# Kernel optimization log

Hardware: AMD Instinct MI355X
Metric: run time of the kernel (lower is better)

The kernel has to match this reference:

```python
import jax, jax.numpy as jnp
import numpy as np

N_NODES = 100000
N_EDGES = 6400000


def setup_inputs() -> dict:
    key = jax.random.key(0)
    k = jax.random.split(key, 5)
    x = jax.random.normal(k[0], (N_NODES, 4), dtype=jnp.float32)
    edge_index = jax.random.randint(k[1], (2, N_EDGES), 0, N_NODES, dtype=jnp.int32)
    # Glorot-style init for GCN linear weights
    W1 = jax.random.normal(k[2], (4, 16), dtype=jnp.float32) * (1.0 / np.sqrt(4.0))
    b1 = jnp.zeros((16,), dtype=jnp.float32)
    W2 = jax.random.normal(k[3], (16, 2), dtype=jnp.float32) * (1.0 / np.sqrt(16.0))
    b2 = jnp.zeros((2,), dtype=jnp.float32)
    return {"x": x, "edge_index": edge_index, "W1": W1, "b1": b1, "W2": W2, "b2": b2}


def _gcn_conv(x, src, dst, deg_inv_sqrt, W, b):
    """One GCNConv layer: linear transform -> symmetric-normalized scatter-add -> bias.

    src, dst already include self-loops; deg_inv_sqrt precomputed on the
    self-loop-augmented graph (matches PyG GCNConv defaults).
    """
    n = x.shape[0]
    h = x @ W                                   # [N, F_out]
    coef = deg_inv_sqrt[src] * deg_inv_sqrt[dst]  # [E+N]
    msg = h[src] * coef[:, None]                # gather + scale, [E+N, F_out]
    out = jax.ops.segment_sum(msg, dst, num_segments=n)  # scatter-add
    return out + b


def reference(x, edge_index, W1, b1, W2, b2):
    n = x.shape[0]
    loop = jnp.arange(n, dtype=edge_index.dtype)
    src = jnp.concatenate([edge_index[0], loop])  # add self-loops
    dst = jnp.concatenate([edge_index[1], loop])
    deg = jax.ops.segment_sum(jnp.ones_like(dst, dtype=x.dtype), dst, num_segments=n)
    deg_inv_sqrt = jnp.where(deg > 0, jax.lax.rsqrt(deg), 0.0)

    h = jax.nn.relu(_gcn_conv(x, src, dst, deg_inv_sqrt, W1, b1))
    return _gcn_conv(h, src, dst, deg_inv_sqrt, W2, b2)
```

## Files before the change

### kernel.cpp

```cpp
#include <hip/hip_runtime.h>

#define TPB 256
#define CSH 10
#define CN 1024
#define NBC_MAX 128
#define STILE 8192
#define EPT (STILE / TPB)

#define B20 1048576
#define S1F 131072.0f
#define S2F 8192.0f

__device__ __forceinline__ unsigned enc_fx(float v, float scale) {
    int xi = __float2int_rn(v * scale);
    xi = max(-(B20 - 1), min(B20 - 1, xi));
    return (unsigned)(xi + B20);
}

__global__ void k_zero(int* __restrict__ p, int n) {
    int i = blockIdx.x * blockDim.x + threadIdx.x;
    if (i < n) p[i] = 0;
}

__global__ void k_histc(const int* __restrict__ dst, int* __restrict__ bcnt, int E, int NBC) {
    __shared__ int cnt[NBC_MAX];
    if (threadIdx.x < NBC_MAX) cnt[threadIdx.x] = 0;
    __syncthreads();
    int per = (E + gridDim.x - 1) / gridDim.x;
    int s = blockIdx.x * per;
    int e = min(E, s + per);
    for (int i = s + threadIdx.x; i < e; i += TPB)
        atomicAdd(&cnt[dst[i] >> CSH], 1);
    __syncthreads();
    if (threadIdx.x < (unsigned)NBC && cnt[threadIdx.x])
        atomicAdd(&bcnt[threadIdx.x], cnt[threadIdx.x]);
}

__global__ void k_scanc(const int* __restrict__ bcnt, int* __restrict__ bbase,
                        int* __restrict__ cursorB, int NBC) {
    __shared__ int sh[NBC_MAX];
    int t = threadIdx.x;
    if (t < NBC) sh[t] = bcnt[t];
    __syncthreads();
    if (t <= NBC) {
        int sum = 0;
        for (int j = 0; j < t && j < NBC; j++) sum += sh[j];
        if (t < NBC) { bbase[t] = sum; cursorB[t] = sum; }
        else if (t == NBC) bbase[NBC] = sum;
    }
}

__global__ void k_passC(const int* __restrict__ src, const int* __restrict__ dst,
                        int* __restrict__ cursorB, unsigned* __restrict__ packed,
                        int E, int NBC, int epb) {
    __shared__ unsigned stage[STILE];
    __shared__ int cnt[NBC_MAX], lb[NBC_MAX], gb[NBC_MAX];
    int bs = blockIdx.x * epb;
    int be = min(E, bs + epb);
    for (int tb = bs; tb < be; tb += STILE) {
        int te = min(be, tb + STILE);
        if (threadIdx.x < NBC_MAX) cnt[threadIdx.x] = 0;
        __syncthreads();
        unsigned pk[EPT];
        int br[EPT];
#pragma unroll
        for (int u = 0; u < EPT; u++) {
            int i = tb + u * TPB + (int)threadIdx.x;
            br[u] = -1;
            if (i < te) {
                int d = dst[i];
                int b = d >> CSH;
                pk[u] = ((unsigned)src[i] << CSH) | (unsigned)(d & (CN - 1));
                int r = atomicAdd(&cnt[b], 1);
                br[u] = b | (r << 7);
            }
        }
        __syncthreads();
        if (threadIdx.x < (unsigned)NBC) {
            int b = threadIdx.x;
            int sum = 0;
            for (int j = 0; j < b; j++) sum += cnt[j];
            lb[b] = sum;
            gb[b] = atomicAdd(&cursorB[b], cnt[b]);
        }
        __syncthreads();
#pragma unroll
        for (int u = 0; u < EPT; u++) {
            if (br[u] >= 0) {
                int b = br[u] & (NBC_MAX - 1);
                int r = br[u] >> 7;
                stage[lb[b] + r] = pk[u];
            }
        }
        __syncthreads();
        int wid = threadIdx.x >> 6, lane = threadIdx.x & 63;
        for (int b = wid; b < NBC; b += 4) {
            int len = cnt[b], l = lb[b], g = gb[b];
            for (int i = lane; i < len; i += 64)
                packed[g + i] = stage[l + i];
        }
        __syncthreads();
    }
}

__global__ void k_degc(const unsigned* __restrict__ packed, const int* __restrict__ bbase,
                       int* __restrict__ deg, int SD, int N) {
    __shared__ int cnt[CN];
    for (int i = threadIdx.x; i < CN; i += TPB) cnt[i] = 0;
    __syncthreads();
    int b = blockIdx.x / SD, s = blockIdx.x - b * SD;
    int e0 = bbase[b], e1 = bbase[b + 1];
    int len = e1 - e0;
    int ce0 = e0 + (int)((long long)len * s / SD);
    int ce1 = e0 + (int)((long long)len * (s + 1) / SD);
    int e = ce0 + threadIdx.x;
    for (; e + 3 * TPB < ce1; e += 4 * TPB) {
        unsigned p0 = packed[e], p1 = packed[e + TPB], p2 = packed[e + 2 * TPB], p3 = packed[e + 3 * TPB];
        atomicAdd(&cnt[p0 & (CN - 1)], 1);
        atomicAdd(&cnt[p1 & (CN - 1)], 1);
        atomicAdd(&cnt[p2 & (CN - 1)], 1);
        atomicAdd(&cnt[p3 & (CN - 1)], 1);
    }
    for (; e < ce1; e += TPB)
        atomicAdd(&cnt[packed[e] & (CN - 1)], 1);
    __syncthreads();
    int node0 = b << CSH;
    for (int i = threadIdx.x; i < CN; i += TPB)
        if (cnt[i] && node0 + i < N) atomicAdd(&deg[node0 + i], cnt[i]);
}

__global__ void k_prepv(const float* __restrict__ x, const int* __restrict__ deg,
                        float* __restrict__ xs, unsigned* __restrict__ xse, int N) {
    int v = blockIdx.x * blockDim.x + threadIdx.x;
    if (v >= N) return;
    float di = rsqrtf((float)(deg[v] + 1));
    float4 xv = ((const float4*)x)[v];
    xv.x *= di; xv.y *= di; xv.z *= di; xv.w *= di;
    ((float4*)xs)[v] = xv;
    uint4 e;
    e.x = enc_fx(xv.x, S1F); e.y = enc_fx(xv.y, S1F);
    e.z = enc_fx(xv.z, S1F); e.w = enc_fx(xv.w, S1F);
    ((uint4*)xse)[v] = e;
}

#define U1 4
__global__ void k_agg1q(const unsigned* __restrict__ packed, const int* __restrict__ bbase,
                        const unsigned* __restrict__ xse,
                        unsigned long long* __restrict__ partial1, int S1) {
    __shared__ unsigned long long acc[CN * 3];
    for (int i = threadIdx.x; i < CN * 3; i += TPB) acc[i] = 0ULL;
    __syncthreads();
    int b = blockIdx.x / S1, s = blockIdx.x - b * S1;
    int e0 = bbase[b], e1 = bbase[b + 1];
    int len = e1 - e0;
    int ce0 = e0 + (int)((long long)len * s / S1);
    int ce1 = e0 + (int)((long long)len * (s + 1) / S1);
    int e = ce0 + threadIdx.x;
    for (; e + (U1 - 1) * TPB < ce1; e += U1 * TPB) {
        unsigned pk[U1];
#pragma unroll
        for (int u = 0; u < U1; u++) pk[u] = packed[e + u * TPB];
        uint4 g[U1];
#pragma unroll
        for (int u = 0; u < U1; u++) g[u] = ((const uint4*)xse)[pk[u] >> CSH];
#pragma unroll
        for (int u = 0; u < U1; u++) {
            int n = pk[u] & (CN - 1);
            unsigned long long v01 = (unsigned long long)g[u].x | ((unsigned long long)g[u].y << 32);
            unsigned long long v23 = (unsigned long long)g[u].z | ((unsigned long long)g[u].w << 32);
            atomicAdd(&acc[n * 3 + 0], v01);
            atomicAdd(&acc[n * 3 + 1], v23);
        }
    }
    for (; e < ce1; e += TPB) {
        unsigned pk = packed[e];
        uint4 g = ((const uint4*)xse)[pk >> CSH];
        int n = pk & (CN - 1);
        atomicAdd(&acc[n * 3 + 0], (unsigned long long)g.x | ((unsigned long long)g.y << 32));
        atomicAdd(&acc[n * 3 + 1], (unsigned long long)g.z | ((unsigned long long)g.w << 32));
    }
    __syncthreads();
    unsigned long long* p = partial1 + (size_t)blockIdx.x * (CN * 2);
    for (int i = threadIdx.x; i < CN * 2; i += TPB)
        p[i] = acc[(i >> 1) * 3 + (i & 1)];
}

__global__ void k_comb1q(const unsigned long long* __restrict__ partial1,
                         const float* __restrict__ xs, const int* __restrict__ deg,
                         const float* __restrict__ W1, const float* __restrict__ b1,
                         const float* __restrict__ W2,
                         float* __restrict__ hs2f, unsigned* __restrict__ hs2e,
                         int S1, int N) {
    __shared__ float w1[64], w2[32], bb[16];
    if (threadIdx.x < 64) w1[threadIdx.x] = W1[threadIdx.x];
    if (threadIdx.x < 32) w2[threadIdx.x] = W2[threadIdx.x];
    if (threadIdx.x < 16) bb[threadIdx.x] = b1[threadIdx.x];
    __syncthreads();
    int v = blockIdx.x * blockDim.x + threadIdx.x;
    if (v >= N) return;
    int b = v >> CSH, lv = v & (CN - 1);
    unsigned long long a01 = 0, a23 = 0;
    for (int s = 0; s < S1; s++) {
        const unsigned long long* q = partial1 + ((size_t)(b * S1 + s) * CN + lv) * 2;
        a01 += q[0];
        a23 += q[1];
    }
    int dg = deg[v];
    long long bias = (long long)dg << 20;
    const float inv = 1.0f / S1F;
    float f0 = (float)((long long)(a01 & 0xffffffffULL) - bias) * inv;
    float f1 = (float)((long long)(a01 >> 32) - bias) * inv;
    float f2 = (float)((long long)(a23 & 0xffffffffULL) - bias) * inv;
    float f3 = (float)((long long)(a23 >> 32) - bias) * inv;
    float4 self = ((const float4*)xs)[v];
    float di = rsqrtf((float)(dg + 1));
    float v0 = (f0 + self.x) * di, v1 = (f1 + self.y) * di;
    float v2 = (f2 + self.z) * di, v3 = (f3 + self.w) * di;
    float s0 = 0.f, s1 = 0.f;
#pragma unroll
    for (int j = 0; j < 16; j++) {
        float h = v0 * w1[j] + v1 * w1[16 + j] + v2 * w1[32 + j] + v3 * w1[48 + j] + bb[j];
        h = fmaxf(h, 0.0f);
        s0 += h * w2[2 * j];
        s1 += h * w2[2 * j + 1];
    }
    s0 *= di; s1 *= di;
    ((float2*)hs2f)[v] = make_float2(s0, s1);
    uint2 e;
    e.x = enc_fx(s0, S2F);
    e.y = enc_fx(s1, S2F);
    ((uint2*)hs2e)[v] = e;
}

#define U2 4
__global__ void k_agg2q(const unsigned* __restrict__ packed, const int* __restrict__ bbase,
                        const unsigned* __restrict__ hs2e,
                        unsigned long long* __restrict__ partial2, int S2) {
    __shared__ unsigned long long acc[CN];
    for (int i = threadIdx.x; i < CN; i += TPB) acc[i] = 0ULL;
    __syncthreads();
    int b = blockIdx.x / S2, s = blockIdx.x - b * S2;
    int e0 = bbase[b], e1 = bbase[b + 1];
    int len = e1 - e0;
    int ce0 = e0 + (int)((long long)len * s / S2);
    int ce1 = e0 + (int)((long long)len * (s + 1) / S2);
    int e = ce0 + threadIdx.x;
    for (; e + (U2 - 1) * TPB < ce1; e += U2 * TPB) {
        unsigned pk[U2];
#pragma unroll
        for (int u = 0; u < U2; u++) pk[u] = packed[e + u * TPB];
        uint2 g[U2];
#pragma unroll
        for (int u = 0; u < U2; u++) g[u] = ((const uint2*)hs2e)[pk[u] >> CSH];
#pragma unroll
        for (int u = 0; u < U2; u++)
            atomicAdd(&acc[pk[u] & (CN - 1)],
                      (unsigned long long)g[u].x | ((unsigned long long)g[u].y << 32));
    }
    for (; e < ce1; e += TPB) {
        unsigned pk = packed[e];
        uint2 g = ((const uint2*)hs2e)[pk >> CSH];
        atomicAdd(&acc[pk & (CN - 1)],
                  (unsigned long long)g.x | ((unsigned long long)g.y << 32));
    }
    __syncthreads();
    unsigned long long* p = partial2 + (size_t)blockIdx.x * CN;
    for (int i = threadIdx.x; i < CN; i += TPB) p[i] = acc[i];
}

__global__ void k_comb2q(const unsigned long long* __restrict__ partial2,
                         const float* __restrict__ hs2f, const int* __restrict__ deg,
                         const float* __restrict__ b2, float* __restrict__ out,
                         int S2, int N) {
    int v = blockIdx.x * blockDim.x + threadIdx.x;
    if (v >= N) return;
    int b = v >> CSH, lv = v & (CN - 1);
    unsigned long long t = 0;
    for (int s = 0; s < S2; s++)
        t += partial2[(size_t)(b * S2 + s) * CN + lv];
    int dg = deg[v];
    long long bias = (long long)dg << 20;
    const float inv = 1.0f / S2F;
    float f0 = (float)((long long)(t & 0xffffffffULL) - bias) * inv;
    float f1 = (float)((long long)(t >> 32) - bias) * inv;
    float2 self = ((const float2*)hs2f)[v];
    float di = rsqrtf((float)(dg + 1));
    ((float2*)out)[v] = make_float2((f0 + self.x) * di + b2[0],
                                    (f1 + self.y) * di + b2[1]);
}


__global__ void k_deg_fb(const int* __restrict__ dst, int* __restrict__ deg, int E) {
    int i = blockIdx.x * blockDim.x + threadIdx.x;
    if (i < E) atomicAdd(&deg[dst[i]], 1);
}
__global__ void k_dis_fb(const int* __restrict__ deg, float* __restrict__ dis, int N) {
    int v = blockIdx.x * blockDim.x + threadIdx.x;
    if (v < N) dis[v] = rsqrtf((float)(deg[v] + 1));
}
__global__ void k_lin1_fb(const float* __restrict__ x, const float* __restrict__ W1,
                          const float* __restrict__ dis, float* __restrict__ hs1,
                          float* __restrict__ agg1, int N) {
    __shared__ float w[64];
    if (threadIdx.x < 64) w[threadIdx.x] = W1[threadIdx.x];
    __syncthreads();
    int v = blockIdx.x * blockDim.x + threadIdx.x;
    if (v >= N) return;
    float4 xv = ((const float4*)x)[v];
    float d = dis[v];
#pragma unroll
    for (int j = 0; j < 16; j++) {
        float h = (xv.x * w[j] + xv.y * w[16 + j] + xv.z * w[32 + j] + xv.w * w[48 + j]) * d;
        hs1[v * 16 + j] = h;
        agg1[v * 16 + j] = h;
    }
}
__global__ void k_scat1_fb(const int* __restrict__ src, const int* __restrict__ dst,
                           const float* __restrict__ hs1, float* __restrict__ agg1, int E4) {
    int t = blockIdx.x * blockDim.x + threadIdx.x;
    if (t >= E4) return;
    int e = t >> 2, q = t & 3;
    int s = src[e], d = dst[e];
    float4 m = ((const float4*)hs1)[s * 4 + q];
    float* a = agg1 + (size_t)d * 16 + q * 4;
    atomicAdd(a + 0, m.x); atomicAdd(a + 1, m.y);
    atomicAdd(a + 2, m.z); atomicAdd(a + 3, m.w);
}
__global__ void k_lin2_fb(const float* __restrict__ agg1, const float* __restrict__ dis,
                          const float* __restrict__ b1, const float* __restrict__ W2,
                          float* __restrict__ hs2, float* __restrict__ agg2, int N) {
    __shared__ float w[32];
    __shared__ float bb[16];
    if (threadIdx.x < 32) w[threadIdx.x] = W2[threadIdx.x];
    if (threadIdx.x < 16) bb[threadIdx.x] = b1[threadIdx.x];
    __syncthreads();
    int v = blockIdx.x * blockDim.x + threadIdx.x;
    if (v >= N) return;
    float d = dis[v];
    float a0 = 0.f, a1 = 0.f;
#pragma unroll
    for (int k = 0; k < 16; k++) {
        float r = fmaxf(agg1[v * 16 + k] * d + bb[k], 0.0f);
        a0 += r * w[k * 2 + 0];
        a1 += r * w[k * 2 + 1];
    }
    float2 hv = make_float2(a0 * d, a1 * d);
    ((float2*)hs2)[v] = hv;
    ((float2*)agg2)[v] = hv;
}
__global__ void k_scat2_fb(const int* __restrict__ src, const int* __restrict__ dst,
                           const float* __restrict__ hs2, float* __restrict__ agg2, int E) {
    int e = blockIdx.x * blockDim.x + threadIdx.x;
    if (e >= E) return;
    int s = src[e], d = dst[e];
    float2 m = ((const float2*)hs2)[s];
    atomicAdd(&agg2[d * 2 + 0], m.x);
    atomicAdd(&agg2[d * 2 + 1], m.y);
}
__global__ void k_out_fb(const float* __restrict__ agg2, const float* __restrict__ dis,
                         const float* __restrict__ b2, float* __restrict__ out, int N) {
    int v = blockIdx.x * blockDim.x + threadIdx.x;
    if (v >= N) return;
    float d = dis[v];
    out[v * 2 + 0] = agg2[v * 2 + 0] * d + b2[0];
    out[v * 2 + 1] = agg2[v * 2 + 1] * d + b2[1];
}


extern "C" void kernel_launch(void* const* d_in, const int* in_sizes, int n_in,
                              void* d_out, int out_size, void* d_ws, size_t ws_size,
                              hipStream_t stream) {
    const float* x  = (const float*)d_in[0];
    const int*   ei = (const int*)d_in[1];
    const float* W1 = (const float*)d_in[2];
    const float* b1 = (const float*)d_in[3];
    const float* W2 = (const float*)d_in[4];
    const float* b2 = (const float*)d_in[5];

    const int N = in_sizes[0] / 4;
    const int E = in_sizes[1] / 2;
    const int* src = ei;
    const int* dst = ei + E;
    float* outp = (float*)d_out;

    auto align = [](size_t v) { return (v + 255) & ~(size_t)255; };
    const int NBC = (N + CN - 1) >> CSH;
    const int gN  = (N + TPB - 1) / TPB;
    const int epb = STILE;
    const int gPC = (E + epb - 1) / epb;
    const int SD = 8;
    const bool src_fits = (size_t)N <= ((size_t)1 << (32 - CSH));
    const bool fx_safe = (long long)E <= (long long)N * 512;

    const int S1 = 8, S2 = 16;
    size_t part_bytes = (size_t)NBC * S1 * CN * 16;
    size_t part2_bytes = (size_t)NBC * S2 * CN * 8;
    size_t part_max = part_bytes > part2_bytes ? part_bytes : part2_bytes;

    size_t need_new = align((size_t)E * 4)
                    + align((size_t)N * 16)
                    + align((size_t)N * 16)
                    + align((size_t)N * 8)
                    + align((size_t)N * 8)
                    + align(((size_t)N + NBC) * 4)
                    + align((size_t)NBC * 4)
                    + align((size_t)(NBC + 1) * 4)
                    + align(part_max);

    if (ws_size >= need_new && NBC <= NBC_MAX && src_fits && fx_safe) {
        char* ws = (char*)d_ws;
        unsigned* packed = (unsigned*)ws; ws += align((size_t)E * 4);
        float* xs    = (float*)ws;    ws += align((size_t)N * 16);
        unsigned* xse = (unsigned*)ws; ws += align((size_t)N * 16);
        float* hs2f  = (float*)ws;    ws += align((size_t)N * 8);
        unsigned* hs2e = (unsigned*)ws; ws += align((size_t)N * 8);
        int* deg     = (int*)ws;      ws += align(((size_t)N + NBC) * 4);
        int* bcnt    = deg + N;
        int* cursorB = (int*)ws;      ws += align((size_t)NBC * 4);
        int* bbase   = (int*)ws;      ws += align((size_t)(NBC + 1) * 4);
        unsigned long long* partial1 = (unsigned long long*)ws;
        unsigned long long* partial2 = (unsigned long long*)ws;

        k_zero<<<(N + NBC + TPB - 1) / TPB, TPB, 0, stream>>>(deg, N + NBC);
        k_histc<<<512, TPB, 0, stream>>>(dst, bcnt, E, NBC);
        k_scanc<<<1, 256, 0, stream>>>(bcnt, bbase, cursorB, NBC);
        k_passC<<<gPC, TPB, 0, stream>>>(src, dst, cursorB, packed, E, NBC, epb);
        k_degc<<<NBC * SD, TPB, 0, stream>>>(packed, bbase, deg, SD, N);
        k_prepv<<<gN, TPB, 0, stream>>>(x, deg, xs, xse, N);
        k_agg1q<<<NBC * S1, TPB, 0, stream>>>(packed, bbase, xse, partial1, S1);
        k_comb1q<<<gN, TPB, 0, stream>>>(partial1, xs, deg, W1, b1, W2, hs2f, hs2e, S1, N);
        k_agg2q<<<NBC * S2, TPB, 0, stream>>>(packed, bbase, hs2e, partial2, S2);
        k_comb2q<<<gN, TPB, 0, stream>>>(partial2, hs2f, deg, b2, outp, S2, N);
    } else {
        char* ws = (char*)d_ws;
        int*   deg  = (int*)ws;   ws += align((size_t)N * 4);
        float* dis  = (float*)ws; ws += align((size_t)N * 4);
        float* hs1  = (float*)ws; ws += align((size_t)N * 16 * 4);
        float* agg1 = (float*)ws; ws += align((size_t)N * 16 * 4);
        float* hs2  = (float*)ws; ws += align((size_t)N * 2 * 4);
        float* agg2 = (float*)ws; ws += align((size_t)N * 2 * 4);
        int gE = (E + TPB - 1) / TPB;
        int gE4 = ((size_t)E * 4 + TPB - 1) / TPB;

        k_zero<<<gN, TPB, 0, stream>>>(deg, N);
        k_deg_fb<<<gE, TPB, 0, stream>>>(dst, deg, E);
        k_dis_fb<<<gN, TPB, 0, stream>>>(deg, dis, N);
        k_lin1_fb<<<gN, TPB, 0, stream>>>(x, W1, dis, hs1, agg1, N);
        k_scat1_fb<<<gE4, TPB, 0, stream>>>(src, dst, hs1, agg1, E * 4);
        k_lin2_fb<<<gN, TPB, 0, stream>>>(agg1, dis, b1, W2, hs2, agg2, N);
        k_scat2_fb<<<gE, TPB, 0, stream>>>(src, dst, hs2, agg2, E);
        k_out_fb<<<gN, TPB, 0, stream>>>(agg2, dis, b2, outp, N);
    }
}
```

Baseline: 244.3 us.

## Replace global bucket sort with per-tile local bucketing and chunk index tables

Drops the global histogram and scan kernels and the atomic global cursors. Each tile of 8192 edges is now sorted by destination bucket only within the tile and written back in place, and the per-tile, per-bucket lengths and offsets are recorded in chunk tables. The degree and aggregation kernels walk these chunk lists per bucket instead of reading one contiguous bucket range, which removes two launches and a serialized pass. In exchange the chunks are short (about 8192/98, roughly 80 edges, per tile and bucket), so the one-wavefront-per-chunk loops leave many lanes idle, reads become scattered, and the old 4-way unrolled loads are gone.

```diff
diff --git a/kernel.cpp b/kernel.cpp
--- a/kernel.cpp
+++ b/kernel.cpp
@@ -11,6 +11,8 @@
 #define S1F 131072.0f
 #define S2F 8192.0f
 
+typedef unsigned long long u64;
+
 __device__ __forceinline__ unsigned enc_fx(float v, float scale) {
     int xi = __float2int_rn(v * scale);
     xi = max(-(B20 - 1), min(B20 - 1, xi));
@@ -22,107 +24,66 @@
     if (i < n) p[i] = 0;
 }
 
-__global__ void k_histc(const int* __restrict__ dst, int* __restrict__ bcnt, int E, int NBC) {
-    __shared__ int cnt[NBC_MAX];
+__global__ void k_passCk(const int* __restrict__ src, const int* __restrict__ dst,
+                         unsigned* __restrict__ packed, int* __restrict__ chunkl,
+                         int* __restrict__ chunkp, int E, int NBC) {
+    __shared__ unsigned stage[STILE];
+    __shared__ int cnt[NBC_MAX], lb[NBC_MAX];
+    int tb = blockIdx.x * STILE;
+    int te = min(E, tb + STILE);
     if (threadIdx.x < NBC_MAX) cnt[threadIdx.x] = 0;
     __syncthreads();
-    int per = (E + gridDim.x - 1) / gridDim.x;
-    int s = blockIdx.x * per;
-    int e = min(E, s + per);
-    for (int i = s + threadIdx.x; i < e; i += TPB)
-        atomicAdd(&cnt[dst[i] >> CSH], 1);
-    __syncthreads();
-    if (threadIdx.x < (unsigned)NBC && cnt[threadIdx.x])
-        atomicAdd(&bcnt[threadIdx.x], cnt[threadIdx.x]);
-}
-
-__global__ void k_scanc(const int* __restrict__ bcnt, int* __restrict__ bbase,
-                        int* __restrict__ cursorB, int NBC) {
-    __shared__ int sh[NBC_MAX];
-    int t = threadIdx.x;
-    if (t < NBC) sh[t] = bcnt[t];
-    __syncthreads();
-    if (t <= NBC) {
+    unsigned pk[EPT];
+    int br[EPT];
+#pragma unroll
+    for (int u = 0; u < EPT; u++) {
+        int i = tb + u * TPB + (int)threadIdx.x;
+        br[u] = -1;
+        if (i < te) {
+            int d = dst[i];
+            int b = d >> CSH;
+            pk[u] = ((unsigned)src[i] << CSH) | (unsigned)(d & (CN - 1));
+            int r = atomicAdd(&cnt[b], 1);
+            br[u] = b | (r << 7);
+        }
+    }
+    __syncthreads();
+    if (threadIdx.x < (unsigned)NBC) {
+        int b = threadIdx.x;
         int sum = 0;
-        for (int j = 0; j < t && j < NBC; j++) sum += sh[j];
-        if (t < NBC) { bbase[t] = sum; cursorB[t] = sum; }
-        else if (t == NBC) bbase[NBC] = sum;
-    }
-}
-
-__global__ void k_passC(const int* __restrict__ src, const int* __restrict__ dst,
-                        int* __restrict__ cursorB, unsigned* __restrict__ packed,
-                        int E, int NBC, int epb) {
-    __shared__ unsigned stage[STILE];
-    __shared__ int cnt[NBC_MAX], lb[NBC_MAX], gb[NBC_MAX];
-    int bs = blockIdx.x * epb;
-    int be = min(E, bs + epb);
-    for (int tb = bs; tb < be; tb += STILE) {
-        int te = min(be, tb + STILE);
-        if (threadIdx.x < NBC_MAX) cnt[threadIdx.x] = 0;
-        __syncthreads();
-        unsigned pk[EPT];
-        int br[EPT];
-#pragma unroll
-        for (int u = 0; u < EPT; u++) {
-            int i = tb + u * TPB + (int)threadIdx.x;
-            br[u] = -1;
-            if (i < te) {
-                int d = dst[i];
-                int b = d >> CSH;
-                pk[u] = ((unsigned)src[i] << CSH) | (unsigned)(d & (CN - 1));
-                int r = atomicAdd(&cnt[b], 1);
-                br[u] = b | (r << 7);
-            }
+        for (int j = 0; j < b; j++) sum += cnt[j];
+        lb[b] = sum;
+        chunkl[blockIdx.x * NBC + b] = cnt[b];
+        chunkp[blockIdx.x * NBC + b] = tb + sum;
+    }
+    __syncthreads();
+#pragma unroll
+    for (int u = 0; u < EPT; u++) {
+        if (br[u] >= 0) {
+            int b = br[u] & (NBC_MAX - 1);
+            stage[lb[b] + (br[u] >> 7)] = pk[u];
         }
-        __syncthreads();
-        if (threadIdx.x < (unsigned)NBC) {
-            int b = threadIdx.x;
-            int sum = 0;
-            for (int j = 0; j < b; j++) sum += cnt[j];
-            lb[b] = sum;
-            gb[b] = atomicAdd(&cursorB[b], cnt[b]);
-        }
-        __syncthreads();
-#pragma unroll
-        for (int u = 0; u < EPT; u++) {
-            if (br[u] >= 0) {
-                int b = br[u] & (NBC_MAX - 1);
-                int r = br[u] >> 7;
-                stage[lb[b] + r] = pk[u];
-            }
-        }
-        __syncthreads();
-        int wid = threadIdx.x >> 6, lane = threadIdx.x & 63;
-        for (int b = wid; b < NBC; b += 4) {
-            int len = cnt[b], l = lb[b], g = gb[b];
-            for (int i = lane; i < len; i += 64)
-                packed[g + i] = stage[l + i];
-        }
-        __syncthreads();
-    }
-}
-
-__global__ void k_degc(const unsigned* __restrict__ packed, const int* __restrict__ bbase,
-                       int* __restrict__ deg, int SD, int N) {
+    }
+    __syncthreads();
+    for (int i = threadIdx.x; i < te - tb; i += TPB)
+        packed[tb + i] = stage[i];
+}
+
+__global__ void k_degk(const unsigned* __restrict__ packed, const int* __restrict__ chunkl,
+                       const int* __restrict__ chunkp, int* __restrict__ deg,
+                       int SD, int ntiles, int NBC, int N) {
     __shared__ int cnt[CN];
     for (int i = threadIdx.x; i < CN; i += TPB) cnt[i] = 0;
     __syncthreads();
     int b = blockIdx.x / SD, s = blockIdx.x - b * SD;
-    int e0 = bbase[b], e1 = bbase[b + 1];
-    int len = e1 - e0;
-    int ce0 = e0 + (int)((long long)len * s / SD);
-    int ce1 = e0 + (int)((long long)len * (s + 1) / SD);
-    int e = ce0 + threadIdx.x;
-    for (; e + 3 * TPB < ce1; e += 4 * TPB) {
-        unsigned p0 = packed[e], p1 = packed[e + TPB], p2 = packed[e + 2 * TPB], p3 = packed[e + 3 * TPB];
-        atomicAdd(&cnt[p0 & (CN - 1)], 1);
-        atomicAdd(&cnt[p1 & (CN - 1)], 1);
-        atomicAdd(&cnt[p2 & (CN - 1)], 1);
-        atomicAdd(&cnt[p3 & (CN - 1)], 1);
-    }
-    for (; e < ce1; e += TPB)
-        atomicAdd(&cnt[packed[e] & (CN - 1)], 1);
+    int wv = threadIdx.x >> 6, lane = threadIdx.x & 63;
+    for (int t = s * 4 + wv; t < ntiles; t += SD * 4) {
+        int len = chunkl[t * NBC + b];
+        if (!len) continue;
+        int pos = chunkp[t * NBC + b];
+        for (int i = lane; i < len; i += 64)
+            atomicAdd(&cnt[packed[pos + i] & (CN - 1)], 1);
+    }
     __syncthreads();
     int node0 = b << CSH;
     for (int i = threadIdx.x; i < CN; i += TPB)
@@ -143,49 +104,33 @@
     ((uint4*)xse)[v] = e;
 }
 
-#define U1 4
-__global__ void k_agg1q(const unsigned* __restrict__ packed, const int* __restrict__ bbase,
-                        const unsigned* __restrict__ xse,
-                        unsigned long long* __restrict__ partial1, int S1) {
-    __shared__ unsigned long long acc[CN * 3];
+__global__ void k_agg1k(const unsigned* __restrict__ packed, const int* __restrict__ chunkl,
+                        const int* __restrict__ chunkp, const unsigned* __restrict__ xse,
+                        u64* __restrict__ partial1, int S1, int ntiles, int NBC) {
+    __shared__ u64 acc[CN * 3];
     for (int i = threadIdx.x; i < CN * 3; i += TPB) acc[i] = 0ULL;
     __syncthreads();
     int b = blockIdx.x / S1, s = blockIdx.x - b * S1;
-    int e0 = bbase[b], e1 = bbase[b + 1];
-    int len = e1 - e0;
-    int ce0 = e0 + (int)((long long)len * s / S1);
-    int ce1 = e0 + (int)((long long)len * (s + 1) / S1);
-    int e = ce0 + threadIdx.x;
-    for (; e + (U1 - 1) * TPB < ce1; e += U1 * TPB) {
-        unsigned pk[U1];
-#pragma unroll
-        for (int u = 0; u < U1; u++) pk[u] = packed[e + u * TPB];
-        uint4 g[U1];
-#pragma unroll
-        for (int u = 0; u < U1; u++) g[u] = ((const uint4*)xse)[pk[u] >> CSH];
-#pragma unroll
-        for (int u = 0; u < U1; u++) {
-            int n = pk[u] & (CN - 1);
-            unsigned long long v01 = (unsigned long long)g[u].x | ((unsigned long long)g[u].y << 32);
-            unsigned long long v23 = (unsigned long long)g[u].z | ((unsigned long long)g[u].w << 32);
-            atomicAdd(&acc[n * 3 + 0], v01);
-            atomicAdd(&acc[n * 3 + 1], v23);
+    int wv = threadIdx.x >> 6, lane = threadIdx.x & 63;
+    for (int t = s * 4 + wv; t < ntiles; t += S1 * 4) {
+        int len = chunkl[t * NBC + b];
+        if (!len) continue;
+        int pos = chunkp[t * NBC + b];
+        for (int i = lane; i < len; i += 64) {
+            unsigned pk = packed[pos + i];
+            uint4 g = ((const uint4*)xse)[pk >> CSH];
+            int n = pk & (CN - 1);
+            atomicAdd(&acc[n * 3 + 0], (u64)g.x | ((u64)g.y << 32));
+            atomicAdd(&acc[n * 3 + 1], (u64)g.z | ((u64)g.w << 32));
         }
     }
-    for (; e < ce1; e += TPB) {
-        unsigned pk = packed[e];
-        uint4 g = ((const uint4*)xse)[pk >> CSH];
-        int n = pk & (CN - 1);
-        atomicAdd(&acc[n * 3 + 0], (unsigned long long)g.x | ((unsigned long long)g.y << 32));
-        atomicAdd(&acc[n * 3 + 1], (unsigned long long)g.z | ((unsigned long long)g.w << 32));
-    }
-    __syncthreads();
-    unsigned long long* p = partial1 + (size_t)blockIdx.x * (CN * 2);
+    __syncthreads();
+    u64* p = partial1 + (size_t)blockIdx.x * (CN * 2);
     for (int i = threadIdx.x; i < CN * 2; i += TPB)
         p[i] = acc[(i >> 1) * 3 + (i & 1)];
 }
 
-__global__ void k_comb1q(const unsigned long long* __restrict__ partial1,
+__global__ void k_comb1q(const u64* __restrict__ partial1,
                          const float* __restrict__ xs, const int* __restrict__ deg,
                          const float* __restrict__ W1, const float* __restrict__ b1,
                          const float* __restrict__ W2,
@@ -199,9 +144,9 @@
     int v = blockIdx.x * blockDim.x + threadIdx.x;
     if (v >= N) return;
     int b = v >> CSH, lv = v & (CN - 1);
-    unsigned long long a01 = 0, a23 = 0;
+    u64 a01 = 0, a23 = 0;
     for (int s = 0; s < S1; s++) {
-        const unsigned long long* q = partial1 + ((size_t)(b * S1 + s) * CN + lv) * 2;
+        const u64* q = partial1 + ((size_t)(b * S1 + s) * CN + lv) * 2;
         a01 += q[0];
         a23 += q[1];
     }
@@ -232,50 +177,37 @@
     ((uint2*)hs2e)[v] = e;
 }
 
-#define U2 4
-__global__ void k_agg2q(const unsigned* __restrict__ packed, const int* __restrict__ bbase,
-                        const unsigned* __restrict__ hs2e,
-                        unsigned long long* __restrict__ partial2, int S2) {
-    __shared__ unsigned long long acc[CN];
+__global__ void k_agg2k(const unsigned* __restrict__ packed, const int* __restrict__ chunkl,
+                        const int* __restrict__ chunkp, const unsigned* __restrict__ hs2e,
+                        u64* __restrict__ partial2, int S2, int ntiles, int NBC) {
+    __shared__ u64 acc[CN];
     for (int i = threadIdx.x; i < CN; i += TPB) acc[i] = 0ULL;
     __syncthreads();
     int b = blockIdx.x / S2, s = blockIdx.x - b * S2;
-    int e0 = bbase[b], e1 = bbase[b + 1];
-    int len = e1 - e0;
-    int ce0 = e0 + (int)((long long)len * s / S2);
-    int ce1 = e0 + (int)((long long)len * (s + 1) / S2);
-    int e = ce0 + threadIdx.x;
-    for (; e + (U2 - 1) * TPB < ce1; e += U2 * TPB) {
-        unsigned pk[U2];
-#pragma unroll
-        for (int u = 0; u < U2; u++) pk[u] = packed[e + u * TPB];
-        uint2 g[U2];
-#pragma unroll
-        for (int u = 0; u < U2; u++) g[u] = ((const uint2*)hs2e)[pk[u] >> CSH];
-#pragma unroll
-        for (int u = 0; u < U2; u++)
-            atomicAdd(&acc[pk[u] & (CN - 1)],
-                      (unsigned long long)g[u].x | ((unsigned long long)g[u].y << 32));
-    }
-    for (; e < ce1; e += TPB) {
-        unsigned pk = packed[e];
-        uint2 g = ((const uint2*)hs2e)[pk >> CSH];
-        atomicAdd(&acc[pk & (CN - 1)],
-                  (unsigned long long)g.x | ((unsigned long long)g.y << 32));
-    }
-    __syncthreads();
-    unsigned long long* p = partial2 + (size_t)blockIdx.x * CN;
+    int wv = threadIdx.x >> 6, lane = threadIdx.x & 63;
+    for (int t = s * 4 + wv; t < ntiles; t += S2 * 4) {
+        int len = chunkl[t * NBC + b];
+        if (!len) continue;
+        int pos = chunkp[t * NBC + b];
+        for (int i = lane; i < len; i += 64) {
+            unsigned pk = packed[pos + i];
+            uint2 g = ((const uint2*)hs2e)[pk >> CSH];
+            atomicAdd(&acc[pk & (CN - 1)], (u64)g.x | ((u64)g.y << 32));
+        }
+    }
+    __syncthreads();
+    u64* p = partial2 + (size_t)blockIdx.x * CN;
     for (int i = threadIdx.x; i < CN; i += TPB) p[i] = acc[i];
 }
 
-__global__ void k_comb2q(const unsigned long long* __restrict__ partial2,
+__global__ void k_comb2q(const u64* __restrict__ partial2,
                          const float* __restrict__ hs2f, const int* __restrict__ deg,
                          const float* __restrict__ b2, float* __restrict__ out,
                          int S2, int N) {
     int v = blockIdx.x * blockDim.x + threadIdx.x;
     if (v >= N) return;
     int b = v >> CSH, lv = v & (CN - 1);
-    unsigned long long t = 0;
+    u64 t = 0;
     for (int s = 0; s < S2; s++)
         t += partial2[(size_t)(b * S2 + s) * CN + lv];
     int dg = deg[v];
@@ -386,14 +318,13 @@
     auto align = [](size_t v) { return (v + 255) & ~(size_t)255; };
     const int NBC = (N + CN - 1) >> CSH;
     const int gN  = (N + TPB - 1) / TPB;
-    const int epb = STILE;
-    const int gPC = (E + epb - 1) / epb;
+    const int ntiles = (E + STILE - 1) / STILE;
     const int SD = 8;
     const bool src_fits = (size_t)N <= ((size_t)1 << (32 - CSH));
     const bool fx_safe = (long long)E <= (long long)N * 512;
 
     const int S1 = 8, S2 = 16;
-    size_t part_bytes = (size_t)NBC * S1 * CN * 16;
+    size_t part_bytes  = (size_t)NBC * S1 * CN * 16;
     size_t part2_bytes = (size_t)NBC * S2 * CN * 8;
     size_t part_max = part_bytes > part2_bytes ? part_bytes : part2_bytes;
 
@@ -402,9 +333,9 @@
                     + align((size_t)N * 16)
                     + align((size_t)N * 8)
                     + align((size_t)N * 8)
-                    + align(((size_t)N + NBC) * 4)
-                    + align((size_t)NBC * 4)
-                    + align((size_t)(NBC + 1) * 4)
+                    + align((size_t)N * 4)
+                    + align((size_t)ntiles * NBC * 4)
+                    + align((size_t)ntiles * NBC * 4)
                     + align(part_max);
 
     if (ws_size >= need_new && NBC <= NBC_MAX && src_fits && fx_safe) {
@@ -414,22 +345,19 @@
         unsigned* xse = (unsigned*)ws; ws += align((size_t)N * 16);
         float* hs2f  = (float*)ws;    ws += align((size_t)N * 8);
         unsigned* hs2e = (unsigned*)ws; ws += align((size_t)N * 8);
-        int* deg     = (int*)ws;      ws += align(((size_t)N + NBC) * 4);
-        int* bcnt    = deg + N;
-        int* cursorB = (int*)ws;      ws += align((size_t)NBC * 4);
-        int* bbase   = (int*)ws;      ws += align((size_t)(NBC + 1) * 4);
-        unsigned long long* partial1 = (unsigned long long*)ws;
-        unsigned long long* partial2 = (unsigned long long*)ws;
-
-        k_zero<<<(N + NBC + TPB - 1) / TPB, TPB, 0, stream>>>(deg, N + NBC);
-        k_histc<<<512, TPB, 0, stream>>>(dst, bcnt, E, NBC);
-        k_scanc<<<1, 256, 0, stream>>>(bcnt, bbase, cursorB, NBC);
-        k_passC<<<gPC, TPB, 0, stream>>>(src, dst, cursorB, packed, E, NBC, epb);
-        k_degc<<<NBC * SD, TPB, 0, stream>>>(packed, bbase, deg, SD, N);
+        int* deg     = (int*)ws;      ws += align((size_t)N * 4);
+        int* chunkl  = (int*)ws;      ws += align((size_t)ntiles * NBC * 4);
+        int* chunkp  = (int*)ws;      ws += align((size_t)ntiles * NBC * 4);
+        u64* partial1 = (u64*)ws;
+        u64* partial2 = (u64*)ws;
+
+        k_zero<<<gN, TPB, 0, stream>>>(deg, N);
+        k_passCk<<<ntiles, TPB, 0, stream>>>(src, dst, packed, chunkl, chunkp, E, NBC);
+        k_degk<<<NBC * SD, TPB, 0, stream>>>(packed, chunkl, chunkp, deg, SD, ntiles, NBC, N);
         k_prepv<<<gN, TPB, 0, stream>>>(x, deg, xs, xse, N);
-        k_agg1q<<<NBC * S1, TPB, 0, stream>>>(packed, bbase, xse, partial1, S1);
+        k_agg1k<<<NBC * S1, TPB, 0, stream>>>(packed, chunkl, chunkp, xse, partial1, S1, ntiles, NBC);
         k_comb1q<<<gN, TPB, 0, stream>>>(partial1, xs, deg, W1, b1, W2, hs2f, hs2e, S1, N);
-        k_agg2q<<<NBC * S2, TPB, 0, stream>>>(packed, bbase, hs2e, partial2, S2);
+        k_agg2k<<<NBC * S2, TPB, 0, stream>>>(packed, chunkl, chunkp, hs2e, partial2, S2, ntiles, NBC);
         k_comb2q<<<gN, TPB, 0, stream>>>(partial2, hs2f, deg, b2, outp, S2, N);
     } else {
         char* ws = (char*)d_ws;
```

Measured after the change: 242.4 us. About the same (-0.7%).
